# Performance work log

Measured on AMD Instinct MI355X. Metric: run time of the kernel, lower is better.

Reference implementation:

```python
import jax, jax.numpy as jnp
import numpy as np

N_EMBD = 768
N_HEAD = 12
HEAD_DIM = N_EMBD // N_HEAD
LN_EPS = 1e-5


def setup_inputs() -> dict:
    key = jax.random.key(0)
    ks = jax.random.split(key, 12)
    s = 0.02
    B, T = 8, 1024
    return {
        "x": jax.random.normal(ks[0], (B, T, N_EMBD), dtype=jnp.float32),
        "ln1_g": jnp.ones((N_EMBD,), jnp.float32),
        "ln1_b": jnp.zeros((N_EMBD,), jnp.float32),
        "w_attn": jax.random.normal(ks[1], (N_EMBD, 3 * N_EMBD), jnp.float32) * s,
        "b_attn": jnp.zeros((3 * N_EMBD,), jnp.float32),
        "w_proj": jax.random.normal(ks[2], (N_EMBD, N_EMBD), jnp.float32) * s,
        "b_proj": jnp.zeros((N_EMBD,), jnp.float32),
        "ln2_g": jnp.ones((N_EMBD,), jnp.float32),
        "ln2_b": jnp.zeros((N_EMBD,), jnp.float32),
        "w_fc1": jax.random.normal(ks[3], (N_EMBD, 4 * N_EMBD), jnp.float32) * s,
        "b_fc1": jnp.zeros((4 * N_EMBD,), jnp.float32),
        "w_fc2": jax.random.normal(ks[4], (4 * N_EMBD, N_EMBD), jnp.float32) * s,
        "b_fc2": jnp.zeros((N_EMBD,), jnp.float32),
    }


def _layernorm(x, g, b):
    mu = jnp.mean(x, axis=-1, keepdims=True)
    var = jnp.mean(jnp.square(x - mu), axis=-1, keepdims=True)
    return (x - mu) * jax.lax.rsqrt(var + LN_EPS) * g + b


def _block(x, ln1_g, ln1_b, w_attn, b_attn, w_proj, b_proj,
           ln2_g, ln2_b, w_fc1, b_fc1, w_fc2, b_fc2):
    B, T, C = x.shape
    # --- causal self-attention (dropout inactive in eval) ---
    h = _layernorm(x, ln1_g, ln1_b)
    qkv = h @ w_attn + b_attn                      # [B,T,3C]
    q, k, v = jnp.split(qkv, 3, axis=-1)
    q = q.reshape(B, T, N_HEAD, HEAD_DIM).transpose(0, 2, 1, 3)  # [B,H,T,D]
    k = k.reshape(B, T, N_HEAD, HEAD_DIM).transpose(0, 2, 1, 3)
    v = v.reshape(B, T, N_HEAD, HEAD_DIM).transpose(0, 2, 1, 3)
    att = jnp.einsum('bhtd,bhsd->bhts', q, k) * (1.0 / np.sqrt(HEAD_DIM))
    mask = jnp.tril(jnp.ones((T, T), dtype=bool))
    att = jnp.where(mask, att, -jnp.inf)
    att = jax.nn.softmax(att, axis=-1)
    y = jnp.einsum('bhts,bhsd->bhtd', att, v)
    y = y.transpose(0, 2, 1, 3).reshape(B, T, C)
    x = x + y @ w_proj + b_proj
    # --- MLP ---
    h2 = _layernorm(x, ln2_g, ln2_b)
    h2 = jax.nn.gelu(h2 @ w_fc1 + b_fc1, approximate=True)
    x = x + h2 @ w_fc2 + b_fc2
    return x


def reference(x, ln1_g, ln1_b, w_attn, b_attn, w_proj, b_proj,
              ln2_g, ln2_b, w_fc1, b_fc1, w_fc2, b_fc2):
    return _block(x, ln1_g, ln1_b, w_attn, b_attn, w_proj, b_proj,
                  ln2_g, ln2_b, w_fc1, b_fc1, w_fc2, b_fc2)
```

## Files before the change

### kernel.cpp

```cpp
#include <hip/hip_runtime.h>
#include <cstdint>
#include <cmath>

typedef unsigned short u16;
typedef __bf16 bf16_t;
typedef bf16_t bf16x8 __attribute__((ext_vector_type(8)));
typedef float f32x4 __attribute__((ext_vector_type(4)));
typedef u16 u16x8 __attribute__((ext_vector_type(8)));
typedef u16 u16x4 __attribute__((ext_vector_type(4)));

#define DEV __device__ __forceinline__

DEV u16 f2b(float f) {
    uint32_t u = __builtin_bit_cast(uint32_t, f);
    u += 0x7FFFu + ((u >> 16) & 1u);
    return (u16)(u >> 16);
}
DEV float b2f(u16 h) { return __builtin_bit_cast(float, (uint32_t)h << 16); }

DEV bf16x8 load8(const u16* p) {
    return __builtin_bit_cast(bf16x8, *reinterpret_cast<const u16x8*>(p));
}

DEV void async16(void* lds, const void* g) {
    __builtin_amdgcn_global_load_lds(
        reinterpret_cast<const __attribute__((address_space(1))) void*>(
            reinterpret_cast<uintptr_t>(g)),
        reinterpret_cast<__attribute__((address_space(3))) void*>(
            reinterpret_cast<uintptr_t>(lds)),
        16, 0, 0);
}

DEV float gelu_t(float x) {
    float z = 0.7978845608028654f * (x + 0.044715f * x * x * x);
    z = fminf(fmaxf(z, -15.0f), 15.0f);
    float e = __expf(2.0f * z);
    return 0.5f * x * (1.0f + (e - 1.0f) / (e + 1.0f));
}

__global__ __launch_bounds__(256) void ln_k(const float* __restrict__ x,
                                            const float* __restrict__ g,
                                            const float* __restrict__ bb,
                                            u16* __restrict__ out) {
    const int lane = threadIdx.x & 63, w = threadIdx.x >> 6;
    const int row = blockIdx.x * 4 + w;
    const float4* xr = reinterpret_cast<const float4*>(x + (size_t)row * 768);
    float4 v[3];
    float s = 0.f, s2 = 0.f;
#pragma unroll
    for (int i = 0; i < 3; ++i) {
        v[i] = xr[i * 64 + lane];
        s += v[i].x + v[i].y + v[i].z + v[i].w;
        s2 += v[i].x * v[i].x + v[i].y * v[i].y + v[i].z * v[i].z + v[i].w * v[i].w;
    }
#pragma unroll
    for (int off = 1; off < 64; off <<= 1) {
        s += __shfl_xor(s, off);
        s2 += __shfl_xor(s2, off);
    }
    const float mu = s * (1.0f / 768.0f);
    const float rstd = rsqrtf(s2 * (1.0f / 768.0f) - mu * mu + 1e-5f);
#pragma unroll
    for (int i = 0; i < 3; ++i) {
        int col = i * 256 + lane * 4;
        u16x4 o;
        o[0] = f2b((v[i].x - mu) * rstd * g[col + 0] + bb[col + 0]);
        o[1] = f2b((v[i].y - mu) * rstd * g[col + 1] + bb[col + 1]);
        o[2] = f2b((v[i].z - mu) * rstd * g[col + 2] + bb[col + 2]);
        o[3] = f2b((v[i].w - mu) * rstd * g[col + 3] + bb[col + 3]);
        *reinterpret_cast<u16x4*>(out + (size_t)row * 768 + col) = o;
    }
}

__global__ __launch_bounds__(256) void wconv_k(const float* __restrict__ W,
                                               u16* __restrict__ WT, int K, int N) {
    __shared__ float tile[32][33];
    const int tx = threadIdx.x, ty = threadIdx.y;
    const int n0 = blockIdx.x * 32, k0 = blockIdx.y * 32;
#pragma unroll
    for (int i = 0; i < 4; ++i)
        tile[ty + i * 8][tx] = W[(size_t)(k0 + ty + i * 8) * N + n0 + tx];
    __syncthreads();
#pragma unroll
    for (int i = 0; i < 4; ++i)
        WT[(size_t)(n0 + ty + i * 8) * K + k0 + tx] = f2b(tile[tx][ty + i * 8]);
}

__global__ __launch_bounds__(256) void vtrans_k(const u16* __restrict__ qkv,
                                                u16* __restrict__ vT) {
    __shared__ u16 tile[32][33];
    const int tx = threadIdx.x, ty = threadIdx.y;
    const int t0 = blockIdx.x * 32, d0 = blockIdx.y * 32, bh = blockIdx.z;
    const int b = bh / 12, hd = bh % 12;
#pragma unroll
    for (int i = 0; i < 4; ++i)
        tile[ty + i * 8][tx] =
            qkv[(size_t)(b * 1024 + t0 + ty + i * 8) * 2304 + 1536 + hd * 64 + d0 + tx];
    __syncthreads();
#pragma unroll
    for (int i = 0; i < 4; ++i)
        vT[(size_t)(bh * 64 + d0 + ty + i * 8) * 1024 + t0 + tx] = tile[tx][ty + i * 8];
}

template <int ACT, int RESID, int OUTBF>
__global__ __launch_bounds__(256) void gemm_bt(const u16* __restrict__ A,
                                               const u16* __restrict__ BT,
                                               const float* __restrict__ bias,
                                               const float* __restrict__ resid,
                                               void* __restrict__ out,
                                               int M, int N, int K) {
    __shared__ u16 As[2][128 * 32];
    __shared__ u16 Bs[2][128 * 32];
    const int tid = threadIdx.x, lane = tid & 63;
    const int l15 = lane & 15, lg = lane >> 4;
    const int mBase = blockIdx.y * 128, nBase = blockIdx.x * 128;
    const int w = tid >> 6, wr = w >> 1, wc = w & 1;

    auto stage = [&](int buf, int kk) {
        const int k0 = kk << 5;
#pragma unroll
        for (int i = 0; i < 2; ++i) {
            int c = i * 256 + tid;
            int row = c >> 2, colE = (c & 3) << 3;
            async16(As[buf] + c * 8, A + (size_t)(mBase + row) * K + k0 + colE);
        }
#pragma unroll
        for (int i = 0; i < 2; ++i) {
            int c = i * 256 + tid;
            int row = c >> 2, colE = (c & 3) << 3;
            async16(Bs[buf] + c * 8, BT + (size_t)(nBase + row) * K + k0 + colE);
        }
    };

    f32x4 acc[4][4] = {};
    const int nsteps = K >> 5;
    stage(0, 0);
    for (int kk = 0; kk < nsteps; ++kk) {
        const int cur = kk & 1;
        if (kk + 1 < nsteps) {
            stage(cur ^ 1, kk + 1);
            asm volatile("s_waitcnt vmcnt(4)" ::: "memory");
        } else {
            asm volatile("s_waitcnt vmcnt(0)" ::: "memory");
        }
        __builtin_amdgcn_s_barrier();
        asm volatile("" ::: "memory");

        bf16x8 af[4], bfr[4];
#pragma unroll
        for (int mi = 0; mi < 4; ++mi)
            af[mi] = load8(As[cur] + (wr * 64 + mi * 16 + l15) * 32 + lg * 8);
#pragma unroll
        for (int ni = 0; ni < 4; ++ni)
            bfr[ni] = load8(Bs[cur] + (wc * 64 + ni * 16 + l15) * 32 + lg * 8);
        __builtin_amdgcn_s_setprio(1);
#pragma unroll
        for (int mi = 0; mi < 4; ++mi)
#pragma unroll
            for (int ni = 0; ni < 4; ++ni)
                acc[mi][ni] = __builtin_amdgcn_mfma_f32_16x16x32_bf16(
                    af[mi], bfr[ni], acc[mi][ni], 0, 0, 0);
        __builtin_amdgcn_s_setprio(0);

        asm volatile("" ::: "memory");
        __builtin_amdgcn_s_barrier();
    }
#pragma unroll
    for (int mi = 0; mi < 4; ++mi) {
#pragma unroll
        for (int ni = 0; ni < 4; ++ni) {
            const int row0 = mBase + wr * 64 + mi * 16 + lg * 4;
            const int col = nBase + wc * 64 + ni * 16 + l15;
            const float bv = bias[col];
#pragma unroll
            for (int r = 0; r < 4; ++r) {
                float v = acc[mi][ni][r] + bv;
                if (ACT == 1) v = gelu_t(v);
                size_t off = (size_t)(row0 + r) * N + col;
                if (RESID) v += resid[off];
                if (OUTBF)
                    ((u16*)out)[off] = f2b(v);
                else
                    ((float*)out)[off] = v;
            }
        }
    }
}

__global__ __launch_bounds__(256, 3) void attn_k(const u16* __restrict__ qkv,
                                                 const u16* __restrict__ vT,
                                                 u16* __restrict__ y) {
    __shared__ u16 Ks[2][64 * 64];
    __shared__ u16 Vs[2][64 * 64];
    __shared__ u16 Ps[4][2][16 * 64];
    const int tid = threadIdx.x, lane = tid & 63, w = tid >> 6;
    const int bid = blockIdx.x;
    const uint32_t permPk = 2u | (7u << 3) | (1u << 6) | (4u << 9) | (6u << 12) |
                            (0u << 15) | (5u << 18) | (3u << 21);
    const int qt = (permPk >> (((bid + (bid >> 8)) & 7) * 3)) & 7;
    const int bh = ((bid >> 8) << 5) + ((bid & 255) >> 3);
    const int b = bh / 12, hd = bh % 12;
    const int l15 = lane & 15, lg = lane >> 4;
    const int r0 = qt * 128 + w * 32;

    const float qscale = 0.125f * 1.4426950408889634f;
    bf16x8 qf[2][2];
#pragma unroll
    for (int m = 0; m < 2; ++m) {
        const u16* qb = qkv + (size_t)(b * 1024 + r0 + m * 16 + l15) * 2304 + hd * 64;
#pragma unroll
        for (int ks = 0; ks < 2; ++ks) {
            u16x8 u = *reinterpret_cast<const u16x8*>(qb + ks * 32 + lg * 8);
            u16x8 o;
#pragma unroll
            for (int jj = 0; jj < 8; ++jj) o[jj] = f2b(b2f(u[jj]) * qscale);
            qf[m][ks] = __builtin_bit_cast(bf16x8, o);
        }
    }

    const u16* kbase = qkv + (size_t)(b * 1024) * 2304 + 768 + hd * 64;
    const u16* vbase = vT + (size_t)(bh * 64) * 1024;

    auto stage = [&](int buf, int j) {
#pragma unroll
        for (int i = 0; i < 2; ++i) {
            int c = i * 256 + tid;
            int row = c >> 3, sc = ((c & 7) ^ (row & 7)) << 3;
            async16(Ks[buf] + c * 8, kbase + (size_t)(j * 64 + row) * 2304 + sc);
        }
#pragma unroll
        for (int i = 0; i < 2; ++i) {
            int c = i * 256 + tid;
            int row = c >> 3, sc = ((c & 7) ^ (row & 7)) << 3;
            async16(Vs[buf] + c * 8, vbase + (size_t)row * 1024 + j * 64 + sc);
        }
    };

    f32x4 oacc[2][4] = {};
    float mrow[2][4], lrow[2][4];
#pragma unroll
    for (int m = 0; m < 2; ++m)
#pragma unroll
        for (int r = 0; r < 4; ++r) {
            mrow[m][r] = -1e30f;
            lrow[m][r] = 0.f;
        }

    const int jd = (r0 + 31) >> 6;
    const int jmax = qt * 2 + 1;

    stage(0, 0);
    for (int j = 0; j <= jmax; ++j) {
        const int cur = j & 1;
        if (j < jmax) {
            stage(cur ^ 1, j + 1);
            asm volatile("s_waitcnt vmcnt(4)" ::: "memory");
        } else {
            asm volatile("s_waitcnt vmcnt(0)" ::: "memory");
        }
        __builtin_amdgcn_s_barrier();
        asm volatile("" ::: "memory");

        if (j <= jd) {
            const bool diag = (j == jd);
            const u16* Kc = Ks[cur];
            const u16* Vc = Vs[cur];
            f32x4 s[2][4] = {};
            __builtin_amdgcn_s_setprio(1);
#pragma unroll
            for (int ks = 0; ks < 2; ++ks) {
                bf16x8 kf[4];
#pragma unroll
                for (int ni = 0; ni < 4; ++ni) {
                    int key = ni * 16 + l15;
                    kf[ni] = load8(Kc + key * 64 + (((ks * 4 + lg) ^ (key & 7)) << 3));
                }
#pragma unroll
                for (int ni = 0; ni < 4; ++ni) {
                    s[0][ni] = __builtin_amdgcn_mfma_f32_16x16x32_bf16(
                        qf[0][ks], kf[ni], s[0][ni], 0, 0, 0);
                    s[1][ni] = __builtin_amdgcn_mfma_f32_16x16x32_bf16(
                        qf[1][ks], kf[ni], s[1][ni], 0, 0, 0);
                }
            }
            __builtin_amdgcn_s_setprio(0);

#pragma unroll
            for (int m = 0; m < 2; ++m) {
                if (diag) {
#pragma unroll
                    for (int ni = 0; ni < 4; ++ni) {
                        int key = j * 64 + ni * 16 + l15;
#pragma unroll
                        for (int r = 0; r < 4; ++r) {
                            int qrow = r0 + m * 16 + lg * 4 + r;
                            if (key > qrow) s[m][ni][r] = -1e30f;
                        }
                    }
                }
                float pmax[4] = {-1e30f, -1e30f, -1e30f, -1e30f};
#pragma unroll
                for (int ni = 0; ni < 4; ++ni)
#pragma unroll
                    for (int r = 0; r < 4; ++r) pmax[r] = fmaxf(pmax[r], s[m][ni][r]);
#pragma unroll
                for (int off = 1; off < 16; off <<= 1)
#pragma unroll
                    for (int r = 0; r < 4; ++r)
                        pmax[r] = fmaxf(pmax[r], __shfl_xor(pmax[r], off));

                float scal[4], psum[4] = {0.f, 0.f, 0.f, 0.f};
#pragma unroll
                for (int r = 0; r < 4; ++r) {
                    float mnew = fmaxf(mrow[m][r], pmax[r]);
                    scal[r] = exp2f(mrow[m][r] - mnew);
                    mrow[m][r] = mnew;
                }
#pragma unroll
                for (int ni = 0; ni < 4; ++ni) {
                    int key = ni * 16 + l15;
#pragma unroll
                    for (int r = 0; r < 4; ++r) {
                        float pv = exp2f(s[m][ni][r] - mrow[m][r]);
                        psum[r] += pv;
                        int row = lg * 4 + r;
                        Ps[w][m][row * 64 +
                                 ((((key >> 3) ^ (row & 7)) << 3) | (key & 7))] = f2b(pv);
                    }
                }
#pragma unroll
                for (int off = 1; off < 16; off <<= 1)
#pragma unroll
                    for (int r = 0; r < 4; ++r) psum[r] += __shfl_xor(psum[r], off);
#pragma unroll
                for (int r = 0; r < 4; ++r) lrow[m][r] = lrow[m][r] * scal[r] + psum[r];
#pragma unroll
                for (int ni = 0; ni < 4; ++ni)
#pragma unroll
                    for (int r = 0; r < 4; ++r) oacc[m][ni][r] *= scal[r];
            }

            __builtin_amdgcn_s_setprio(1);
#pragma unroll
            for (int ks = 0; ks < 2; ++ks) {
                bf16x8 pf0 =
                    load8(&Ps[w][0][l15 * 64 + (((ks * 4 + lg) ^ (l15 & 7)) << 3)]);
                bf16x8 pf1 =
                    load8(&Ps[w][1][l15 * 64 + (((ks * 4 + lg) ^ (l15 & 7)) << 3)]);
                bf16x8 vf[4];
#pragma unroll
                for (int ni = 0; ni < 4; ++ni) {
                    int d = ni * 16 + l15;
                    vf[ni] = load8(Vc + d * 64 + (((ks * 4 + lg) ^ (d & 7)) << 3));
                }
#pragma unroll
                for (int ni = 0; ni < 4; ++ni) {
                    oacc[0][ni] = __builtin_amdgcn_mfma_f32_16x16x32_bf16(
                        pf0, vf[ni], oacc[0][ni], 0, 0, 0);
                    oacc[1][ni] = __builtin_amdgcn_mfma_f32_16x16x32_bf16(
                        pf1, vf[ni], oacc[1][ni], 0, 0, 0);
                }
            }
            __builtin_amdgcn_s_setprio(0);
        }
        asm volatile("" ::: "memory");
        __builtin_amdgcn_s_barrier();
        asm volatile("" ::: "memory");
    }

#pragma unroll
    for (int m = 0; m < 2; ++m) {
        float rl[4];
#pragma unroll
        for (int r = 0; r < 4; ++r) rl[r] = 1.0f / lrow[m][r];
#pragma unroll
        for (int ni = 0; ni < 4; ++ni) {
            int col = hd * 64 + ni * 16 + l15;
#pragma unroll
            for (int r = 0; r < 4; ++r) {
                int row = r0 + m * 16 + lg * 4 + r;
                y[(size_t)(b * 1024 + row) * 768 + col] = f2b(oacc[m][ni][r] * rl[r]);
            }
        }
    }
}

extern "C" void kernel_launch(void* const* d_in, const int* in_sizes, int n_in,
                              void* d_out, int out_size, void* d_ws, size_t ws_size,
                              hipStream_t stream) {
    const float* x      = (const float*)d_in[0];
    const float* ln1_g  = (const float*)d_in[1];
    const float* ln1_b  = (const float*)d_in[2];
    const float* w_attn = (const float*)d_in[3];
    const float* b_attn = (const float*)d_in[4];
    const float* w_proj = (const float*)d_in[5];
    const float* b_proj = (const float*)d_in[6];
    const float* ln2_g  = (const float*)d_in[7];
    const float* ln2_b  = (const float*)d_in[8];
    const float* w_fc1  = (const float*)d_in[9];
    const float* b_fc1  = (const float*)d_in[10];
    const float* w_fc2  = (const float*)d_in[11];
    const float* b_fc2  = (const float*)d_in[12];
    float* out = (float*)d_out;

    char* p = (char*)d_ws;
    auto take = [&](size_t n) {
        char* r = p;
        p += (n + 255) & ~(size_t)255;
        return r;
    };
    u16* wT_attn = (u16*)take((size_t)2304 * 768 * 2);
    u16* wT_proj = (u16*)take((size_t)768 * 768 * 2);
    u16* wT_fc1  = (u16*)take((size_t)3072 * 768 * 2);
    u16* wT_fc2  = (u16*)take((size_t)768 * 3072 * 2);
    u16* h       = (u16*)take((size_t)8192 * 768 * 2);
    u16* bufA    = (u16*)take((size_t)50331648);
    u16* yb      = (u16*)take((size_t)8192 * 768 * 2);
    float* x1    = (float*)take((size_t)8192 * 768 * 4);
    u16* qkv = bufA;
    u16* vT  = bufA + (size_t)8192 * 2304;
    u16* g1  = bufA;

    const dim3 tb(32, 8);
    wconv_k<<<dim3(2304 / 32, 768 / 32), tb, 0, stream>>>(w_attn, wT_attn, 768, 2304);
    wconv_k<<<dim3(768 / 32, 768 / 32), tb, 0, stream>>>(w_proj, wT_proj, 768, 768);
    wconv_k<<<dim3(3072 / 32, 768 / 32), tb, 0, stream>>>(w_fc1, wT_fc1, 768, 3072);
    wconv_k<<<dim3(768 / 32, 3072 / 32), tb, 0, stream>>>(w_fc2, wT_fc2, 3072, 768);
    ln_k<<<2048, 256, 0, stream>>>(x, ln1_g, ln1_b, h);
    gemm_bt<0, 0, 1><<<dim3(18, 64), 256, 0, stream>>>(h, wT_attn, b_attn, nullptr,
                                                       qkv, 8192, 2304, 768);
    vtrans_k<<<dim3(32, 2, 96), tb, 0, stream>>>(qkv, vT);
    attn_k<<<768, 256, 0, stream>>>(qkv, vT, yb);
    gemm_bt<0, 1, 0><<<dim3(6, 64), 256, 0, stream>>>(yb, wT_proj, b_proj, x,
                                                      x1, 8192, 768, 768);
    ln_k<<<2048, 256, 0, stream>>>(x1, ln2_g, ln2_b, h);
    gemm_bt<1, 0, 1><<<dim3(24, 64), 256, 0, stream>>>(h, wT_fc1, b_fc1, nullptr,
                                                       g1, 8192, 3072, 768);
    gemm_bt<0, 1, 0><<<dim3(6, 64), 256, 0, stream>>>(g1, wT_fc2, b_fc2, x1,
                                                      out, 8192, 768, 3072);
}
```

Before: 296.9 us.

## Triple-buffer GEMM loads, swizzle block order, and transpose attention score layout

New measurement: 260.4 us. 12.3% less time.

```diff
diff --git a/kernel.cpp b/kernel.cpp
--- a/kernel.cpp
+++ b/kernel.cpp
@@ -109,11 +109,15 @@
                                                const float* __restrict__ resid,
                                                void* __restrict__ out,
                                                int M, int N, int K) {
-    __shared__ u16 As[2][128 * 32];
-    __shared__ u16 Bs[2][128 * 32];
+    __shared__ u16 As[3][128 * 32];
+    __shared__ u16 Bs[3][128 * 32];
     const int tid = threadIdx.x, lane = tid & 63;
     const int l15 = lane & 15, lg = lane >> 4;
-    const int mBase = blockIdx.y * 128, nBase = blockIdx.x * 128;
+    const int nx = gridDim.x;
+    const int bid = blockIdx.y * nx + blockIdx.x;
+    const int q = (nx * gridDim.y) >> 3;
+    const int swz = (bid & 7) * q + (bid >> 3);
+    const int mBase = (swz / nx) * 128, nBase = (swz % nx) * 128;
     const int w = tid >> 6, wr = w >> 1, wc = w & 1;
 
     auto stage = [&](int buf, int kk) {
@@ -135,10 +139,15 @@
     f32x4 acc[4][4] = {};
     const int nsteps = K >> 5;
     stage(0, 0);
+    stage(1, 1);
+    int cur = 0;
     for (int kk = 0; kk < nsteps; ++kk) {
-        const int cur = kk & 1;
-        if (kk + 1 < nsteps) {
-            stage(cur ^ 1, kk + 1);
+        if (kk + 2 < nsteps) {
+            int nb = cur + 2;
+            if (nb >= 3) nb -= 3;
+            stage(nb, kk + 2);
+            asm volatile("s_waitcnt vmcnt(8)" ::: "memory");
+        } else if (kk + 1 < nsteps) {
             asm volatile("s_waitcnt vmcnt(4)" ::: "memory");
         } else {
             asm volatile("s_waitcnt vmcnt(0)" ::: "memory");
@@ -164,6 +173,7 @@
 
         asm volatile("" ::: "memory");
         __builtin_amdgcn_s_barrier();
+        cur = (cur == 2) ? 0 : cur + 1;
     }
 #pragma unroll
     for (int mi = 0; mi < 4; ++mi) {
@@ -237,14 +247,8 @@
     };
 
     f32x4 oacc[2][4] = {};
-    float mrow[2][4], lrow[2][4];
-#pragma unroll
-    for (int m = 0; m < 2; ++m)
-#pragma unroll
-        for (int r = 0; r < 4; ++r) {
-            mrow[m][r] = -1e30f;
-            lrow[m][r] = 0.f;
-        }
+    float mrow[2] = {-1e30f, -1e30f};
+    float lrow[2] = {0.f, 0.f};
 
     const int jd = (r0 + 31) >> 6;
     const int jmax = qt * 2 + 1;
@@ -278,9 +282,9 @@
 #pragma unroll
                 for (int ni = 0; ni < 4; ++ni) {
                     s[0][ni] = __builtin_amdgcn_mfma_f32_16x16x32_bf16(
-                        qf[0][ks], kf[ni], s[0][ni], 0, 0, 0);
+                        kf[ni], qf[0][ks], s[0][ni], 0, 0, 0);
                     s[1][ni] = __builtin_amdgcn_mfma_f32_16x16x32_bf16(
-                        qf[1][ks], kf[ni], s[1][ni], 0, 0, 0);
+                        kf[ni], qf[1][ks], s[1][ni], 0, 0, 0);
                 }
             }
             __builtin_amdgcn_s_setprio(0);
@@ -288,65 +292,61 @@
 #pragma unroll
             for (int m = 0; m < 2; ++m) {
                 if (diag) {
+                    const int qrow = r0 + m * 16 + l15;
 #pragma unroll
                     for (int ni = 0; ni < 4; ++ni) {
-                        int key = j * 64 + ni * 16 + l15;
-#pragma unroll
-                        for (int r = 0; r < 4; ++r) {
-                            int qrow = r0 + m * 16 + lg * 4 + r;
-                            if (key > qrow) s[m][ni][r] = -1e30f;
-                        }
+                        int key = j * 64 + ni * 16 + lg * 4;
+#pragma unroll
+                        for (int r = 0; r < 4; ++r)
+                            if (key + r > qrow) s[m][ni][r] = -1e30f;
                     }
                 }
-                float pmax[4] = {-1e30f, -1e30f, -1e30f, -1e30f};
+                float pmax = -1e30f;
 #pragma unroll
                 for (int ni = 0; ni < 4; ++ni)
 #pragma unroll
-                    for (int r = 0; r < 4; ++r) pmax[r] = fmaxf(pmax[r], s[m][ni][r]);
-#pragma unroll
-                for (int off = 1; off < 16; off <<= 1)
-#pragma unroll
-                    for (int r = 0; r < 4; ++r)
-                        pmax[r] = fmaxf(pmax[r], __shfl_xor(pmax[r], off));
-
-                float scal[4], psum[4] = {0.f, 0.f, 0.f, 0.f};
-#pragma unroll
-                for (int r = 0; r < 4; ++r) {
-                    float mnew = fmaxf(mrow[m][r], pmax[r]);
-                    scal[r] = exp2f(mrow[m][r] - mnew);
-                    mrow[m][r] = mnew;
-                }
+                    for (int r = 0; r < 4; ++r) pmax = fmaxf(pmax, s[m][ni][r]);
+                pmax = fmaxf(pmax, __shfl_xor(pmax, 16));
+                pmax = fmaxf(pmax, __shfl_xor(pmax, 32));
+
+                if (!__all(pmax <= mrow[m] + 8.0f)) {
+                    float mnew = fmaxf(mrow[m], pmax);
+                    float scal = exp2f(mrow[m] - mnew);
+                    mrow[m] = mnew;
+                    lrow[m] *= scal;
+#pragma unroll
+                    for (int r = 0; r < 4; ++r) {
+                        float sr = __shfl(scal, lg * 4 + r);
+#pragma unroll
+                        for (int ni = 0; ni < 4; ++ni) oacc[m][ni][r] *= sr;
+                    }
+                }
+                float psum = 0.f;
 #pragma unroll
                 for (int ni = 0; ni < 4; ++ni) {
-                    int key = ni * 16 + l15;
+                    u16x4 pk;
 #pragma unroll
                     for (int r = 0; r < 4; ++r) {
-                        float pv = exp2f(s[m][ni][r] - mrow[m][r]);
-                        psum[r] += pv;
-                        int row = lg * 4 + r;
-                        Ps[w][m][row * 64 +
-                                 ((((key >> 3) ^ (row & 7)) << 3) | (key & 7))] = f2b(pv);
+                        float pv = exp2f(s[m][ni][r] - mrow[m]);
+                        psum += pv;
+                        pk[r] = f2b(pv);
                     }
-                }
-#pragma unroll
-                for (int off = 1; off < 16; off <<= 1)
-#pragma unroll
-                    for (int r = 0; r < 4; ++r) psum[r] += __shfl_xor(psum[r], off);
-#pragma unroll
-                for (int r = 0; r < 4; ++r) lrow[m][r] = lrow[m][r] * scal[r] + psum[r];
-#pragma unroll
-                for (int ni = 0; ni < 4; ++ni)
-#pragma unroll
-                    for (int r = 0; r < 4; ++r) oacc[m][ni][r] *= scal[r];
+                    *reinterpret_cast<u16x4*>(
+                        &Ps[w][m][l15 * 64 + ((ni * 16 + lg * 4) ^ ((l15 & 7) << 3))]) =
+                        pk;
+                }
+                psum += __shfl_xor(psum, 16);
+                psum += __shfl_xor(psum, 32);
+                lrow[m] += psum;
             }
 
             __builtin_amdgcn_s_setprio(1);
 #pragma unroll
             for (int ks = 0; ks < 2; ++ks) {
-                bf16x8 pf0 =
-                    load8(&Ps[w][0][l15 * 64 + (((ks * 4 + lg) ^ (l15 & 7)) << 3)]);
-                bf16x8 pf1 =
-                    load8(&Ps[w][1][l15 * 64 + (((ks * 4 + lg) ^ (l15 & 7)) << 3)]);
+                bf16x8 pf0 = load8(
+                    &Ps[w][0][l15 * 64 + ((ks * 32 + lg * 8) ^ ((l15 & 7) << 3))]);
+                bf16x8 pf1 = load8(
+                    &Ps[w][1][l15 * 64 + ((ks * 32 + lg * 8) ^ ((l15 & 7) << 3))]);
                 bf16x8 vf[4];
 #pragma unroll
                 for (int ni = 0; ni < 4; ++ni) {
@@ -370,16 +370,14 @@
 
 #pragma unroll
     for (int m = 0; m < 2; ++m) {
-        float rl[4];
-#pragma unroll
-        for (int r = 0; r < 4; ++r) rl[r] = 1.0f / lrow[m][r];
-#pragma unroll
-        for (int ni = 0; ni < 4; ++ni) {
-            int col = hd * 64 + ni * 16 + l15;
-#pragma unroll
-            for (int r = 0; r < 4; ++r) {
-                int row = r0 + m * 16 + lg * 4 + r;
-                y[(size_t)(b * 1024 + row) * 768 + col] = f2b(oacc[m][ni][r] * rl[r]);
+#pragma unroll
+        for (int r = 0; r < 4; ++r) {
+            float rl = 1.0f / __shfl(lrow[m], lg * 4 + r);
+            int row = r0 + m * 16 + lg * 4 + r;
+#pragma unroll
+            for (int ni = 0; ni < 4; ++ni) {
+                int col = hd * 64 + ni * 16 + l15;
+                y[(size_t)(b * 1024 + row) * 768 + col] = f2b(oacc[m][ni][r] * rl);
             }
         }
     }
```
